# Performance work log

Hardware: AMD Instinct MI355X
Metric: run time of the kernel (lower is better)

The kernel has to match this reference:

```python
import jax, jax.numpy as jnp
import numpy as np


def setup_inputs() -> dict:
    key = jax.random.key(0)
    ks = jax.random.split(key, 14)
    N, D, H, L, K = 16384, 1024, 1024, 256, 4096
    s = 0.02  # small init scale for stable activations
    return {
        "x": jax.random.uniform(ks[0], (N, D), dtype=jnp.float32),
        "embed_pool": jax.random.normal(ks[1], (K, L), dtype=jnp.float32),
        "ew1": jax.random.normal(ks[2], (D, H), dtype=jnp.float32) * s,
        "eb1": jnp.zeros((H,), jnp.float32),
        "ew2": jax.random.normal(ks[3], (H, H), dtype=jnp.float32) * s,
        "eb2": jnp.zeros((H,), jnp.float32),
        "ew3": jax.random.normal(ks[4], (H, L), dtype=jnp.float32) * s,
        "eb3": jnp.zeros((L,), jnp.float32),
        "dw1": jax.random.normal(ks[5], (L, H), dtype=jnp.float32) * s,
        "db1": jnp.zeros((H,), jnp.float32),
        "dw2": jax.random.normal(ks[6], (H, H), dtype=jnp.float32) * s,
        "db2": jnp.zeros((H,), jnp.float32),
        "dw3": jax.random.normal(ks[7], (H, D), dtype=jnp.float32) * s,
        "db3": jnp.zeros((D,), jnp.float32),
    }


def _gelu(t):
    # torch nn.GELU default = exact erf gelu
    return jax.nn.gelu(t, approximate=False)


def reference(x, embed_pool, ew1, eb1, ew2, eb2, ew3, eb3, dw1, db1, dw2, db2, dw3, db3):
    sg = jax.lax.stop_gradient
    # encoder (Dropout is identity at eval)
    h = _gelu(x @ ew1 + eb1)
    h = _gelu(h @ ew2 + eb2)
    z_e = h @ ew3 + eb3  # [N, L]
    # vectorized nearest-neighbor codebook search (argmin of ||z_e - e_k||)
    # squared distances via expansion; argmin identical to argmin of norms
    d2 = (jnp.sum(z_e * z_e, axis=1, keepdims=True)
          - 2.0 * (z_e @ embed_pool.T)
          + jnp.sum(embed_pool * embed_pool, axis=1))  # [N, K]
    z_index = jnp.argmin(d2, axis=1)  # [N]
    z_discrete = jax.nn.one_hot(z_index, embed_pool.shape[0], dtype=jnp.int32)
    z_q = embed_pool[z_index]  # [N, L]
    # straight-through estimator
    z_ss = z_e - sg(z_e) + sg(z_q)
    # decoder
    h = _gelu(z_ss @ dw1 + db1)
    h = _gelu(h @ dw2 + db2)
    x_pred = jax.nn.sigmoid(h @ dw3 + db3)  # [N, D]
    loss = (jnp.sum((x - x_pred) ** 2)
            + jnp.sum((sg(z_e) - z_q) ** 2)
            + 0.25 * jnp.sum((z_e - sg(z_q)) ** 2)) / x.shape[0]
    return x_pred, z_discrete, loss
```

## Files before the change

### kernel.cpp

```cpp
#include <hip/hip_runtime.h>
#include <math.h>


#define MB (1024ULL * 1024ULL)

typedef __attribute__((ext_vector_type(8))) short s16x8;
typedef __attribute__((ext_vector_type(4))) float f32x4;

__device__ __forceinline__ ushort f2bf(float f) {
    unsigned u = __float_as_uint(f);
    u += 0x7fffu + ((u >> 16) & 1u);
    return (ushort)(u >> 16);
}
__device__ __forceinline__ float bf2f(ushort h) {
    return __uint_as_float(((unsigned)h) << 16);
}
__device__ __forceinline__ float gelu_f(float v) {
    return 0.5f * v * (1.0f + erff(v * 0.70710678118654752f));
}
__device__ __forceinline__ void gload16(const void* g, void* l) {
    __builtin_amdgcn_global_load_lds(
        (const __attribute__((address_space(1))) void*)g,
        (__attribute__((address_space(3))) void*)l, 16, 0, 0);
}

__device__ __forceinline__ void conv_body(const float* __restrict__ in,
                                          ushort* __restrict__ out,
                                          int n8, int vb, int nB)
{
    for (int i = vb * 256 + threadIdx.x; i < n8; i += nB * 256) {
        const float4 v0 = *(const float4*)(in + (size_t)i * 8);
        const float4 v1 = *(const float4*)(in + (size_t)i * 8 + 4);
        s16x8 h;
        h[0] = f2bf(v0.x); h[1] = f2bf(v0.y); h[2] = f2bf(v0.z); h[3] = f2bf(v0.w);
        h[4] = f2bf(v1.x); h[5] = f2bf(v1.y); h[6] = f2bf(v1.z); h[7] = f2bf(v1.w);
        *(s16x8*)(out + (size_t)i * 8) = h;
    }
}

__global__ __launch_bounds__(256)
void prep_all(const float* __restrict__ x, ushort* __restrict__ xb,
              const float* __restrict__ pool, ushort* __restrict__ poolb,
              float* __restrict__ cn,
              const float* __restrict__ ew1, ushort* __restrict__ w1,
              const float* __restrict__ ew2, ushort* __restrict__ w2,
              const float* __restrict__ ew3, ushort* __restrict__ w3,
              const float* __restrict__ dw1, ushort* __restrict__ v1,
              const float* __restrict__ dw2, ushort* __restrict__ v2,
              const float* __restrict__ dw3, ushort* __restrict__ v3)
{
    __shared__ float tile[32][33];
    const int b = blockIdx.x;
    const int tid = threadIdx.x;

    if (b < 2048) {
        conv_body(x, xb, 16384 * 1024 / 8, b, 2048);
        return;
    }
    if (b < 2560) {
        conv_body(pool, poolb, 4096 * 256 / 8, b - 2048, 512);
        return;
    }
    if (b < 3584) {
        const int r = (b - 2560) * 4 + (tid >> 6);
        const int lane = tid & 63;
        float4 v = *(const float4*)(pool + (size_t)r * 256 + lane * 4);
        float s = v.x * v.x + v.y * v.y + v.z * v.z + v.w * v.w;
        #pragma unroll
        for (int o = 32; o > 0; o >>= 1) s += __shfl_down(s, o);
        if (lane == 0) cn[r] = s;
        return;
    }

    const float* in; ushort* out; int Kd, Nn, vb;
    if (b < 4608)      { in = ew1; out = w1; Kd = 1024; Nn = 1024; vb = b - 3584; }
    else if (b < 5632) { in = ew2; out = w2; Kd = 1024; Nn = 1024; vb = b - 4608; }
    else if (b < 5888) { in = ew3; out = w3; Kd = 1024; Nn = 256;  vb = b - 5632; }
    else if (b < 6144) { in = dw1; out = v1; Kd = 256;  Nn = 1024; vb = b - 5888; }
    else if (b < 7168) { in = dw2; out = v2; Kd = 1024; Nn = 1024; vb = b - 6144; }
    else               { in = dw3; out = v3; Kd = 1024; Nn = 1024; vb = b - 7168; }

    const int nxw = Nn / 32;
    const int n0 = (vb % nxw) * 32, k0 = (vb / nxw) * 32;
    const int tx = tid & 31, ty = tid >> 5;
    #pragma unroll
    for (int r = 0; r < 4; r++)
        tile[ty + r * 8][tx] = in[(size_t)(k0 + ty + r * 8) * Nn + n0 + tx];
    __syncthreads();
    #pragma unroll
    for (int r = 0; r < 4; r++) {
        const float v = tile[tx][ty + r * 8];
        out[(size_t)(n0 + ty + r * 8) * Kd + k0 + tx] = f2bf(v);
    }
}

template<int EPI>
__global__ __launch_bounds__(512, 2)
void gemm_big(const ushort* __restrict__ A, const ushort* __restrict__ B,
              const float* __restrict__ bias, int Kd, int Nn,
              ushort* __restrict__ Cu,
              float* __restrict__ pval, int* __restrict__ pidx,
              float* __restrict__ zd)
{
    extern __shared__ ushort smem[];
    constexpr int BUFS = 512 * 64;

    const int tid = threadIdx.x;
    const int wave = tid >> 6, lane = tid & 63;

    const int nx = gridDim.x;
    const int nwg = nx * gridDim.y;
    const int orig = blockIdx.y * nx + blockIdx.x;
    const int wgid = (orig & 7) * (nwg >> 3) + (orig >> 3);
    const int bx = wgid % nx, by = wgid / nx;

    const int m0 = by * 256, n0 = bx * 256;
    const int wr = wave >> 2, wc = wave & 3;
    const int fcol = lane & 15, kgrp = lane >> 4;
    const int NT = Kd / 64;
    const int rs = Kd * 2;

    const int srow = lane >> 3;
    const int sswz = ((lane & 7) ^ srow) << 4;
    const char* Abase = (const char*)A + (size_t)m0 * rs;
    const char* Bbase = (const char*)B + (size_t)n0 * rs;

    f32x4 acc[8][4];
    #pragma unroll
    for (int m = 0; m < 8; m++)
        #pragma unroll
        for (int n = 0; n < 4; n++)
            acc[m][n] = (f32x4){0.f, 0.f, 0.f, 0.f};

    auto STAGE = [&](int buf, int t) {
        ushort* dst = smem + buf * BUFS;
        const size_t kb = (size_t)t * 128;
        #pragma unroll
        for (int g = 0; g < 4; g++) {
            const int rb = g * 64 + wave * 8;
            gload16(Abase + (size_t)(rb + srow) * rs + kb + sswz, dst + rb * 64);
            gload16(Bbase + (size_t)(rb + srow) * rs + kb + sswz,
                    dst + (256 + rb) * 64);
        }
    };
    auto LD = [&](int buf, int r, int u) -> s16x8 {
        return *(const s16x8*)(smem + buf * BUFS + r * 64 + ((u ^ (r & 7)) << 3));
    };

    STAGE(0, 0);
    for (int t = 0; t < NT; ++t) {
        asm volatile("s_waitcnt vmcnt(0)" ::: "memory");
        __builtin_amdgcn_s_barrier();
        if (t + 1 < NT) STAGE((t + 1) & 1, t + 1);
        const int buf = t & 1;
        s16x8 b2[4][2];
        #pragma unroll
        for (int n = 0; n < 4; n++) {
            const int r = 256 + wc * 64 + n * 16 + fcol;
            #pragma unroll
            for (int ks = 0; ks < 2; ks++) b2[n][ks] = LD(buf, r, ks * 4 + kgrp);
        }
        #pragma unroll
        for (int h = 0; h < 2; h++) {
            s16x8 a2[4][2];
            #pragma unroll
            for (int i = 0; i < 4; i++) {
                const int r = wr * 128 + (h * 4 + i) * 16 + fcol;
                #pragma unroll
                for (int ks = 0; ks < 2; ks++) a2[i][ks] = LD(buf, r, ks * 4 + kgrp);
            }
            __builtin_amdgcn_s_setprio(1);
            #pragma unroll
            for (int i = 0; i < 4; i++)
                #pragma unroll
                for (int n = 0; n < 4; n++)
                    #pragma unroll
                    for (int ks = 0; ks < 2; ks++)
                        acc[h * 4 + i][n] = __builtin_amdgcn_mfma_f32_16x16x32_bf16(
                            a2[i][ks], b2[n][ks], acc[h * 4 + i][n], 0, 0, 0);
            __builtin_amdgcn_s_setprio(0);
        }
    }
    __builtin_amdgcn_sched_barrier(0);

    int colg[4];
    float bcol[4];
    #pragma unroll
    for (int n = 0; n < 4; n++) {
        colg[n] = n0 + wc * 64 + n * 16 + fcol;
        bcol[n] = bias[colg[n]];
    }

    if constexpr (EPI == 1) {
        #pragma unroll
        for (int m = 0; m < 8; m++)
            #pragma unroll
            for (int v = 0; v < 4; v++) {
                const int row = m0 + wr * 128 + m * 16 + kgrp * 4 + v;
                #pragma unroll
                for (int n = 0; n < 4; n++) {
                    float val = gelu_f(acc[m][n][v] + bcol[n]);
                    Cu[(size_t)row * Nn + colg[n]] = f2bf(val);
                }
            }
    } else if constexpr (EPI == 3) {
        __syncthreads();
        float* sv = (float*)smem;
        int*   si = (int*)(sv + 1024);
        #pragma unroll
        for (int m = 0; m < 8; m++)
            #pragma unroll
            for (int v = 0; v < 4; v++) {
                float best = INFINITY;
                int bidx = 0x7fffffff;
                #pragma unroll
                for (int n = 0; n < 4; n++) {
                    float sc = bcol[n] - 2.0f * acc[m][n][v];
                    if (sc < best || (sc == best && colg[n] < bidx)) { best = sc; bidx = colg[n]; }
                }
                #pragma unroll
                for (int d = 1; d < 16; d <<= 1) {
                    float ov = __shfl_xor(best, d, 64);
                    int   oi = __shfl_xor(bidx, d, 64);
                    if (ov < best || (ov == best && oi < bidx)) { best = ov; bidx = oi; }
                }
                if (fcol == 0) {
                    const int rl = wr * 128 + m * 16 + kgrp * 4 + v;
                    sv[wc * 256 + rl] = best;
                    si[wc * 256 + rl] = bidx;
                }
            }
        __syncthreads();
        if (tid < 256) {
            float v0 = sv[tid];
            int   i0 = si[tid];
            #pragma unroll
            for (int c = 1; c < 4; c++) {
                float v1 = sv[c * 256 + tid];
                int   i1 = si[c * 256 + tid];
                if (v1 < v0 || (v1 == v0 && i1 < i0)) { v0 = v1; i0 = i1; }
            }
            pval[(size_t)(m0 + tid) * nx + bx] = v0;
            pidx[(size_t)(m0 + tid) * nx + bx] = i0;
        }
        const int lrow = tid >> 6;
        const int cseg = (tid & 63) * 4;
        const f32x4 z4 = (f32x4){0.f, 0.f, 0.f, 0.f};
        #pragma unroll
        for (int p = 0; p < 32; p++) {
            float* zp = zd + (size_t)(m0 + p * 8 + lrow) * Nn + n0 + cseg;
            __builtin_nontemporal_store(z4, (f32x4*)zp);
        }
    }
}

template<int EPI>
__global__ __launch_bounds__(512, 2)
void gemm_128(const ushort* __restrict__ A, const ushort* __restrict__ B,
              const float* __restrict__ bias, int Kd, int Nn,
              ushort* __restrict__ Cu, float* __restrict__ Cf)
{
    extern __shared__ ushort smem[];
    constexpr int BUFS = 256 * 64;

    const int tid = threadIdx.x;
    const int wave = tid >> 6, lane = tid & 63;

    const int nx = gridDim.x;
    const int nwg = nx * gridDim.y;
    const int orig = blockIdx.y * nx + blockIdx.x;
    const int wgid = (orig & 7) * (nwg >> 3) + (orig >> 3);
    const int bx = wgid % nx, by = wgid / nx;

    const int m0 = by * 128, n0 = bx * 128;
    const int wr = wave >> 2, wc = wave & 3;
    const int fcol = lane & 15, kgrp = lane >> 4;
    const int NT = Kd / 64;
    const int rs = Kd * 2;

    const int srow = lane >> 3;
    const int sswz = ((lane & 7) ^ srow) << 4;
    const char* Abase = (const char*)A + (size_t)m0 * rs;
    const char* Bbase = (const char*)B + (size_t)n0 * rs;

    f32x4 acc[4][2];
    #pragma unroll
    for (int m = 0; m < 4; m++)
        #pragma unroll
        for (int n = 0; n < 2; n++)
            acc[m][n] = (f32x4){0.f, 0.f, 0.f, 0.f};

    auto STAGE = [&](int buf, int t) {
        ushort* dst = smem + buf * BUFS;
        const size_t kb = (size_t)t * 128;
        #pragma unroll
        for (int g = 0; g < 2; g++) {
            const int rb = g * 64 + wave * 8;
            gload16(Abase + (size_t)(rb + srow) * rs + kb + sswz, dst + rb * 64);
            gload16(Bbase + (size_t)(rb + srow) * rs + kb + sswz,
                    dst + (128 + rb) * 64);
        }
    };
    auto LD = [&](int buf, int r, int u) -> s16x8 {
        return *(const s16x8*)(smem + buf * BUFS + r * 64 + ((u ^ (r & 7)) << 3));
    };

    STAGE(0, 0);
    STAGE(1, 1);
    for (int t = 0; t < NT; ++t) {
        if (t + 1 < NT) asm volatile("s_waitcnt vmcnt(4)" ::: "memory");
        else            asm volatile("s_waitcnt vmcnt(0)" ::: "memory");
        __builtin_amdgcn_s_barrier();
        if (t + 2 < NT) STAGE((t + 2) % 3, t + 2);
        const int buf = t % 3;
        s16x8 a2[4][2], b2[2][2];
        #pragma unroll
        for (int m = 0; m < 4; m++) {
            const int r = wr * 64 + m * 16 + fcol;
            #pragma unroll
            for (int ks = 0; ks < 2; ks++) a2[m][ks] = LD(buf, r, ks * 4 + kgrp);
        }
        #pragma unroll
        for (int n = 0; n < 2; n++) {
            const int r = 128 + wc * 32 + n * 16 + fcol;
            #pragma unroll
            for (int ks = 0; ks < 2; ks++) b2[n][ks] = LD(buf, r, ks * 4 + kgrp);
        }
        __builtin_amdgcn_s_setprio(1);
        #pragma unroll
        for (int m = 0; m < 4; m++)
            #pragma unroll
            for (int n = 0; n < 2; n++)
                #pragma unroll
                for (int ks = 0; ks < 2; ks++)
                    acc[m][n] = __builtin_amdgcn_mfma_f32_16x16x32_bf16(
                        a2[m][ks], b2[n][ks], acc[m][n], 0, 0, 0);
        __builtin_amdgcn_s_setprio(0);
    }
    __builtin_amdgcn_sched_barrier(0);

    #pragma unroll
    for (int n = 0; n < 2; n++) {
        const int col = n0 + wc * 32 + n * 16 + fcol;
        const float bc = bias[col];
        #pragma unroll
        for (int m = 0; m < 4; m++)
            #pragma unroll
            for (int v = 0; v < 4; v++) {
                const int row = m0 + wr * 64 + m * 16 + kgrp * 4 + v;
                float val = acc[m][n][v] + bc;
                if constexpr (EPI == 0) {
                    Cu[(size_t)row * Nn + col] = f2bf(val);
                } else if constexpr (EPI == 1) {
                    Cu[(size_t)row * Nn + col] = f2bf(gelu_f(val));
                } else {
                    Cf[(size_t)row * Nn + col] = 1.0f / (1.0f + expf(-val));
                }
            }
    }
}

__global__ __launch_bounds__(256)
void argmin_gather(const float* __restrict__ pval, const int* __restrict__ pidx,
                   int nblk, const ushort* __restrict__ zE,
                   const float* __restrict__ pool,
                   float* __restrict__ zdisc,
                   const float* __restrict__ xpT, const float* __restrict__ x,
                   float* __restrict__ xpred,
                   float* __restrict__ vqP, float* __restrict__ sseP)
{
    const int t = threadIdx.x;
    const int r = blockIdx.x * 4 + (t >> 6);
    const int l = t & 63;

    float best = INFINITY;
    int bi = 0x7fffffff;
    if (l < nblk) {
        best = pval[(size_t)r * nblk + l];
        bi = pidx[(size_t)r * nblk + l];
    }
    #pragma unroll
    for (int d = 32; d > 0; d >>= 1) {
        float ov = __shfl_xor(best, d, 64);
        int   oi = __shfl_xor(bi, d, 64);
        if (ov < best || (ov == best && oi < bi)) { best = ov; bi = oi; }
    }
    const int kbest = bi;

    if (l == 0) zdisc[(size_t)r * 4096 + kbest] = 1.0f;

    const float4 pz = *(const float4*)(pool + (size_t)kbest * 256 + l * 4);
    const ushort4 zh = *(const ushort4*)(zE + (size_t)r * 256 + l * 4);
    float d0 = bf2f(zh.x) - pz.x;
    float d1 = bf2f(zh.y) - pz.y;
    float d2 = bf2f(zh.z) - pz.z;
    float d3 = bf2f(zh.w) - pz.w;
    float svq = d0 * d0 + d1 * d1 + d2 * d2 + d3 * d3;

    const float* src = xpT + (size_t)kbest * 1024;
    const float* xr  = x + (size_t)r * 1024;
    float* dst = xpred + (size_t)r * 1024;
    float s = 0.0f;
    #pragma unroll
    for (int j = 0; j < 4; j++) {
        const int c = (j * 64 + l) * 4;
        f32x4 v = *(const f32x4*)(src + c);
        const float4 xv = *(const float4*)(xr + c);
        __builtin_nontemporal_store(v, (f32x4*)(dst + c));
        float e0 = xv.x - v[0], e1 = xv.y - v[1];
        float e2 = xv.z - v[2], e3 = xv.w - v[3];
        s += e0 * e0 + e1 * e1 + e2 * e2 + e3 * e3;
    }
    #pragma unroll
    for (int o = 32; o > 0; o >>= 1) {
        s   += __shfl_xor(s, o, 64);
        svq += __shfl_xor(svq, o, 64);
    }
    if (l == 0) { sseP[r] = s; vqP[r] = svq; }
}

__global__ __launch_bounds__(256)
void loss_final(const float* __restrict__ sseP, int nP,
                const float* __restrict__ vqP, int nV,
                float* __restrict__ out)
{
    int tid = threadIdx.x;
    float sx = 0.0f, svq = 0.0f;
    for (int i = tid; i < nP; i += 256) sx += sseP[i];
    for (int i = tid; i < nV; i += 256) svq += vqP[i];
    __shared__ float a[256], b[256];
    a[tid] = sx; b[tid] = svq;
    __syncthreads();
    for (int s = 128; s > 0; s >>= 1) {
        if (tid < s) { a[tid] += a[tid + s]; b[tid] += b[tid + s]; }
        __syncthreads();
    }
    if (tid == 0) out[0] = (a[0] + 1.25f * b[0]) / 16384.0f;
}

extern "C" void kernel_launch(void* const* d_in, const int* in_sizes, int n_in,
                              void* d_out, int out_size, void* d_ws, size_t ws_size,
                              hipStream_t stream)
{
    const float* x    = (const float*)d_in[0];
    const float* pool = (const float*)d_in[1];
    const float* ew1  = (const float*)d_in[2];
    const float* eb1  = (const float*)d_in[3];
    const float* ew2  = (const float*)d_in[4];
    const float* eb2  = (const float*)d_in[5];
    const float* ew3  = (const float*)d_in[6];
    const float* eb3  = (const float*)d_in[7];
    const float* dw1  = (const float*)d_in[8];
    const float* db1  = (const float*)d_in[9];
    const float* dw2  = (const float*)d_in[10];
    const float* db2  = (const float*)d_in[11];
    const float* dw3  = (const float*)d_in[12];
    const float* db3  = (const float*)d_in[13];

    const int N = 16384, D = 1024, H = 1024, L = 256, K = 4096;

    float* out   = (float*)d_out;
    float* xpred = out;
    float* zdisc = out + (size_t)N * D;
    float* lossp = zdisc + (size_t)N * K;

    char* ws = (char*)d_ws;
    ushort* xb    = (ushort*)(ws + 0 * MB);
    ushort* h1    = (ushort*)(ws + 32 * MB);
    ushort* h2    = (ushort*)(ws + 64 * MB);
    ushort* zE    = (ushort*)(ws + 96 * MB);
    ushort* poolb = (ushort*)(ws + 104 * MB);
    ushort* w1    = (ushort*)(ws + 106 * MB);
    ushort* w2    = (ushort*)(ws + 108 * MB);
    ushort* w3    = (ushort*)(ws + 110 * MB);
    ushort* v1    = (ushort*)(ws + 111 * MB);
    ushort* v2    = (ushort*)(ws + 112 * MB);
    ushort* v3    = (ushort*)(ws + 114 * MB);
    ushort* t3    = (ushort*)(ws + 116 * MB);
    ushort* t4    = (ushort*)(ws + 124 * MB);
    float*  xpT   = (float*)(ws + 132 * MB);
    float*  cn    = (float*)(ws + 148 * MB);
    float*  pv    = (float*)(ws + 149 * MB);
    int*    pi    = (int*)(ws + 150 * MB);
    float*  vqP   = (float*)(ws + 151 * MB);
    float*  sxP   = (float*)(ws + 152 * MB);

    const int SH_BIG = 2 * (512 * 64) * 2;
    const int SH_128 = 3 * (256 * 64) * 2;
    (void)hipFuncSetAttribute((const void*)gemm_big<1>,
        hipFuncAttributeMaxDynamicSharedMemorySize, SH_BIG);
    (void)hipFuncSetAttribute((const void*)gemm_big<3>,
        hipFuncAttributeMaxDynamicSharedMemorySize, SH_BIG);
    (void)hipFuncSetAttribute((const void*)gemm_128<0>,
        hipFuncAttributeMaxDynamicSharedMemorySize, SH_128);
    (void)hipFuncSetAttribute((const void*)gemm_128<1>,
        hipFuncAttributeMaxDynamicSharedMemorySize, SH_128);
    (void)hipFuncSetAttribute((const void*)gemm_128<2>,
        hipFuncAttributeMaxDynamicSharedMemorySize, SH_128);

    dim3 blk(256), gblk(512);

    prep_all<<<8192, blk, 0, stream>>>(x, xb, pool, poolb, cn,
                                       ew1, w1, ew2, w2, ew3, w3,
                                       dw1, v1, dw2, v2, dw3, v3);

    gemm_128<1><<<dim3(H / 128, K / 128), gblk, SH_128, stream>>>(
        poolb, v1, db1, L, H, t3, nullptr);
    gemm_128<1><<<dim3(H / 128, K / 128), gblk, SH_128, stream>>>(
        t3, v2, db2, H, H, t4, nullptr);
    gemm_128<2><<<dim3(D / 128, K / 128), gblk, SH_128, stream>>>(
        t4, v3, db3, H, D, nullptr, xpT);

    gemm_big<1><<<dim3(H / 256, N / 256), gblk, SH_BIG, stream>>>(
        xb, w1, eb1, D, H, h1, nullptr, nullptr, nullptr);
    gemm_big<1><<<dim3(H / 256, N / 256), gblk, SH_BIG, stream>>>(
        h1, w2, eb2, H, H, h2, nullptr, nullptr, nullptr);
    gemm_128<0><<<dim3(L / 128, N / 128), gblk, SH_128, stream>>>(
        h2, w3, eb3, H, L, zE, nullptr);

    gemm_big<3><<<dim3(K / 256, N / 256), gblk, SH_BIG, stream>>>(
        zE, poolb, cn, L, K, nullptr, pv, pi, zdisc);

    argmin_gather<<<N / 4, blk, 0, stream>>>(pv, pi, K / 256, zE, pool,
                                             zdisc, xpT, x, xpred, vqP, sxP);

    loss_final<<<1, blk, 0, stream>>>(sxP, N, vqP, N, lossp);
}
```

Measured before the change: 353.5 us.

## Merge independent encoder and codebook-decoder GEMMs into combined dual-body launches

Pairs each encoder GEMM with the independent decoder-on-codebook GEMM at the same depth and runs both in one grid, dispatching by block index to the 256-tile or 128-tile body. This cuts the GEMM launch count from seven to four and lets the small decoder GEMMs fill idle CUs alongside the large encoder GEMMs, reducing tail effects and launch gaps. The cost is that the merged kernels use the larger shared-memory footprint and the register pressure of both bodies, which may lower occupancy for the 128-tile blocks.

```diff
diff --git a/kernel.cpp b/kernel.cpp
--- a/kernel.cpp
+++ b/kernel.cpp
@@ -95,23 +95,20 @@
 }
 
 template<int EPI>
-__global__ __launch_bounds__(512, 2)
-void gemm_big(const ushort* __restrict__ A, const ushort* __restrict__ B,
-              const float* __restrict__ bias, int Kd, int Nn,
-              ushort* __restrict__ Cu,
-              float* __restrict__ pval, int* __restrict__ pidx,
-              float* __restrict__ zd)
-{
-    extern __shared__ ushort smem[];
+__device__ __forceinline__ void big_body(
+    ushort* smem, int bflat, int nx, int ny,
+    const ushort* __restrict__ A, const ushort* __restrict__ B,
+    const float* __restrict__ bias, int Kd, int Nn,
+    ushort* __restrict__ Cu,
+    float* __restrict__ pval, int* __restrict__ pidx, float* __restrict__ zd)
+{
     constexpr int BUFS = 512 * 64;
 
     const int tid = threadIdx.x;
     const int wave = tid >> 6, lane = tid & 63;
 
-    const int nx = gridDim.x;
-    const int nwg = nx * gridDim.y;
-    const int orig = blockIdx.y * nx + blockIdx.x;
-    const int wgid = (orig & 7) * (nwg >> 3) + (orig >> 3);
+    const int nwg = nx * ny;
+    const int wgid = (bflat & 7) * (nwg >> 3) + (bflat >> 3);
     const int bx = wgid % nx, by = wgid / nx;
 
     const int m0 = by * 256, n0 = bx * 256;
@@ -255,21 +252,19 @@
 }
 
 template<int EPI>
-__global__ __launch_bounds__(512, 2)
-void gemm_128(const ushort* __restrict__ A, const ushort* __restrict__ B,
-              const float* __restrict__ bias, int Kd, int Nn,
-              ushort* __restrict__ Cu, float* __restrict__ Cf)
-{
-    extern __shared__ ushort smem[];
+__device__ __forceinline__ void s128_body(
+    ushort* smem, int bflat, int nx, int ny,
+    const ushort* __restrict__ A, const ushort* __restrict__ B,
+    const float* __restrict__ bias, int Kd, int Nn,
+    ushort* __restrict__ Cu, float* __restrict__ Cf)
+{
     constexpr int BUFS = 256 * 64;
 
     const int tid = threadIdx.x;
     const int wave = tid >> 6, lane = tid & 63;
 
-    const int nx = gridDim.x;
-    const int nwg = nx * gridDim.y;
-    const int orig = blockIdx.y * nx + blockIdx.x;
-    const int wgid = (orig & 7) * (nwg >> 3) + (orig >> 3);
+    const int nwg = nx * ny;
+    const int wgid = (bflat & 7) * (nwg >> 3) + (bflat >> 3);
     const int bx = wgid % nx, by = wgid / nx;
 
     const int m0 = by * 128, n0 = bx * 128;
@@ -358,6 +353,48 @@
                 }
             }
     }
+}
+
+__global__ __launch_bounds__(512, 2)
+void gemm_dual_b1(const ushort* Ab, const ushort* Bb, const float* biasb,
+                  int Kdb, int Nnb, ushort* Cub, int nxb, int nyb,
+                  const ushort* As, const ushort* Bs, const float* biass,
+                  int Kds, int Nns, ushort* Cus, int nxs, int nys)
+{
+    extern __shared__ ushort smem[];
+    const int nbig = nxb * nyb;
+    if ((int)blockIdx.x < nbig)
+        big_body<1>(smem, blockIdx.x, nxb, nyb, Ab, Bb, biasb, Kdb, Nnb, Cub,
+                    nullptr, nullptr, nullptr);
+    else
+        s128_body<1>(smem, blockIdx.x - nbig, nxs, nys, As, Bs, biass,
+                     Kds, Nns, Cus, nullptr);
+}
+
+__global__ __launch_bounds__(512, 2)
+void gemm_dual_128(const ushort* A0, const ushort* B0, const float* bias0,
+                   int Kd0, int Nn0, ushort* Cu0, int nx0, int ny0,
+                   const ushort* A1, const ushort* B1, const float* bias1,
+                   int Kd1, int Nn1, float* Cf1, int nx1, int ny1)
+{
+    extern __shared__ ushort smem[];
+    const int n0 = nx0 * ny0;
+    if ((int)blockIdx.x < n0)
+        s128_body<0>(smem, blockIdx.x, nx0, ny0, A0, B0, bias0, Kd0, Nn0,
+                     Cu0, nullptr);
+    else
+        s128_body<2>(smem, blockIdx.x - n0, nx1, ny1, A1, B1, bias1,
+                     Kd1, Nn1, nullptr, Cf1);
+}
+
+__global__ __launch_bounds__(512, 2)
+void gemm_scores(const ushort* A, const ushort* B, const float* bias,
+                 int Kd, int Nn, int nx, int ny,
+                 float* pval, int* pidx, float* zd)
+{
+    extern __shared__ ushort smem[];
+    big_body<3>(smem, blockIdx.x, nx, ny, A, B, bias, Kd, Nn,
+                nullptr, pval, pidx, zd);
 }
 
 __global__ __launch_bounds__(256)
@@ -487,16 +524,12 @@
 
     const int SH_BIG = 2 * (512 * 64) * 2;
     const int SH_128 = 3 * (256 * 64) * 2;
-    (void)hipFuncSetAttribute((const void*)gemm_big<1>,
+    (void)hipFuncSetAttribute((const void*)gemm_dual_b1,
         hipFuncAttributeMaxDynamicSharedMemorySize, SH_BIG);
-    (void)hipFuncSetAttribute((const void*)gemm_big<3>,
+    (void)hipFuncSetAttribute((const void*)gemm_dual_128,
+        hipFuncAttributeMaxDynamicSharedMemorySize, SH_128);
+    (void)hipFuncSetAttribute((const void*)gemm_scores,
         hipFuncAttributeMaxDynamicSharedMemorySize, SH_BIG);
-    (void)hipFuncSetAttribute((const void*)gemm_128<0>,
-        hipFuncAttributeMaxDynamicSharedMemorySize, SH_128);
-    (void)hipFuncSetAttribute((const void*)gemm_128<1>,
-        hipFuncAttributeMaxDynamicSharedMemorySize, SH_128);
-    (void)hipFuncSetAttribute((const void*)gemm_128<2>,
-        hipFuncAttributeMaxDynamicSharedMemorySize, SH_128);
 
     dim3 blk(256), gblk(512);
 
@@ -504,22 +537,20 @@
                                        ew1, w1, ew2, w2, ew3, w3,
                                        dw1, v1, dw2, v2, dw3, v3);
 
-    gemm_128<1><<<dim3(H / 128, K / 128), gblk, SH_128, stream>>>(
-        poolb, v1, db1, L, H, t3, nullptr);
-    gemm_128<1><<<dim3(H / 128, K / 128), gblk, SH_128, stream>>>(
-        t3, v2, db2, H, H, t4, nullptr);
-    gemm_128<2><<<dim3(D / 128, K / 128), gblk, SH_128, stream>>>(
-        t4, v3, db3, H, D, nullptr, xpT);
-
-    gemm_big<1><<<dim3(H / 256, N / 256), gblk, SH_BIG, stream>>>(
-        xb, w1, eb1, D, H, h1, nullptr, nullptr, nullptr);
-    gemm_big<1><<<dim3(H / 256, N / 256), gblk, SH_BIG, stream>>>(
-        h1, w2, eb2, H, H, h2, nullptr, nullptr, nullptr);
-    gemm_128<0><<<dim3(L / 128, N / 128), gblk, SH_128, stream>>>(
-        h2, w3, eb3, H, L, zE, nullptr);
-
-    gemm_big<3><<<dim3(K / 256, N / 256), gblk, SH_BIG, stream>>>(
-        zE, poolb, cn, L, K, nullptr, pv, pi, zdisc);
+    gemm_dual_b1<<<512, gblk, SH_BIG, stream>>>(
+        xb, w1, eb1, D, H, h1, H / 256, N / 256,
+        poolb, v1, db1, L, H, t3, H / 128, K / 128);
+
+    gemm_dual_b1<<<512, gblk, SH_BIG, stream>>>(
+        h1, w2, eb2, H, H, h2, H / 256, N / 256,
+        t3, v2, db2, H, H, t4, H / 128, K / 128);
+
+    gemm_dual_128<<<512, gblk, SH_128, stream>>>(
+        h2, w3, eb3, H, L, zE, L / 128, N / 128,
+        t4, v3, db3, H, D, xpT, D / 128, K / 128);
+
+    gemm_scores<<<(K / 256) * (N / 256), gblk, SH_BIG, stream>>>(
+        zE, poolb, cn, L, K, K / 256, N / 256, pv, pi, zdisc);
 
     argmin_gather<<<N / 4, blk, 0, stream>>>(pv, pi, K / 256, zE, pool,
                                              zdisc, xpT, x, xpred, vqP, sxP);
```

Measured after the change: 340.3 us. 1.04x faster.
